# Optimization experiments

Hardware: AMD Instinct MI355X
Metric: run time of the kernel (lower is better)

Reference implementation:

```python
import jax, jax.numpy as jnp
import numpy as np

B, N, K, D, H, L = 2, 2048, 256, 768, 256, 64
REL_PROP = 3
NUM_BUCKETS = 64


def _pair_scores(u, dist_feat, left_w, left_b, right_w, right_b, out_w, out_b):
    # OptFFpairs-style pairwise scorer: left(u)_i + right(u)_j + dist_emb -> relu -> out
    left = jnp.einsum('bkd,hd->bkh', u, left_w) + left_b    # [B,K,H]
    right = jnp.einsum('bkd,hd->bkh', u, right_w) + right_b  # [B,K,H]
    h = jax.nn.relu(left[:, :, None, :] + right[:, None, :, :] + dist_feat)  # [B,K,K,H]
    return jnp.einsum('bijh,lh->bijl', h, out_w) + out_b     # [B,K,K,L]


def setup_inputs():
    key = jax.random.key(0)
    ks = jax.random.split(key, 12)
    s = 0.02
    all_span_vecs = jax.random.normal(ks[0], (B, N, D), dtype=jnp.float32)
    span_vecs = jax.random.normal(ks[1], (B, K, D), dtype=jnp.float32)
    span_begin = jnp.sort(jax.random.randint(ks[2], (B, K), 0, 1000), axis=-1).astype(jnp.int32)
    span_end = (span_begin + jax.random.randint(ks[3], (B, K), 1, 16)).astype(jnp.int32)
    square_mask = jnp.ones((B, K, K), dtype=jnp.float32)
    span_lengths = jnp.full((B,), float(K), dtype=jnp.float32)
    prune_indices = jnp.stack([
        jnp.sort(jax.random.choice(jax.random.fold_in(ks[4], b), N, (K,), replace=False))
        for b in range(B)
    ]).astype(jnp.int32)
    return {
        'all_span_vecs': all_span_vecs, 'span_vecs': span_vecs,
        'span_begin': span_begin, 'span_end': span_end,
        'square_mask': square_mask, 'span_lengths': span_lengths,
        'prune_indices': prune_indices,
        'left_w': jax.random.normal(ks[5], (H, D)) * s, 'left_b': jnp.zeros((H,), jnp.float32),
        'right_w': jax.random.normal(ks[6], (H, D)) * s, 'right_b': jnp.zeros((H,), jnp.float32),
        'dist_emb': jax.random.normal(ks[7], (NUM_BUCKETS, H)) * s,
        'out_w': jax.random.normal(ks[8], (L, H)) * s, 'out_b': jnp.zeros((L,), jnp.float32),
        'A_w': jax.random.normal(ks[9], (D, L)) * s,
        'B_w': jax.random.normal(ks[10], (D, L)) * s,
        'gate_w': jax.random.normal(ks[11], (D, 2 * D)) * s, 'gate_b': jnp.zeros((D,), jnp.float32),
    }


def reference(all_span_vecs, span_vecs, span_begin, span_end, square_mask, span_lengths,
              prune_indices, left_w, left_b, right_w, right_b, dist_emb, out_w, out_b,
              A_w, B_w, gate_w, gate_b):
    # distance-bucket embedding of the span pair (span_pair_generator)
    dist = span_begin[:, None, :] - span_end[:, :, None]                 # [B,K,K]
    buckets = jnp.clip(jnp.abs(dist), 0, NUM_BUCKETS - 1)
    dist_feat = dist_emb[buckets]                                        # [B,K,K,H]
    inv_len = 1.0 / span_lengths[:, None, None]                          # [B,1,1]

    update = span_vecs
    scores = _pair_scores(update, dist_feat, left_w, left_b, right_w, right_b, out_w, out_b)
    for _ in range(REL_PROP):
        probs = jax.nn.sigmoid(scores) * square_mask[..., None]          # [B,K,K,L]
        # torch: (A(probs) * update.unsqueeze(-2)).sum(-3) -> sum over i (rows)
        ctxt1 = jnp.einsum('bijl,dl,bid->bjd', probs, A_w, update) * inv_len
        # torch: (B(probs) * update.unsqueeze(-3)).sum(-2) -> sum over j (cols)
        ctxt2 = jnp.einsum('bijl,dl,bjd->bid', probs, B_w, update) * inv_len
        c = ctxt1 + ctxt2
        # MyGate: sigmoid-gated convex combination of old state and context
        g = jax.nn.sigmoid(jnp.concatenate([update, c], axis=-1) @ gate_w.T + gate_b)
        update = g * update + (1.0 - g) * c
        scores = _pair_scores(update, dist_feat, left_w, left_b, right_w, right_b, out_w, out_b)

    # overwrite_spans: scatter updated filtered spans back into the full span tensor
    valid = jnp.arange(K)[None, :] < span_lengths[:, None]               # [B,K]
    old = jnp.take_along_axis(all_span_vecs, prune_indices[..., None], axis=1)
    vals = jnp.where(valid[..., None], update, old)
    bidx = jnp.arange(B)[:, None]
    new_all = all_span_vecs.at[bidx, prune_indices].set(vals)
    return new_all, update, scores
```

## Files before the change

### kernel.cpp

```cpp
#include <hip/hip_runtime.h>

#define B_ 2
#define N_ 2048
#define K_ 256
#define D_ 768
#define H_ 256
#define L_ 64
#define BK_ (B_*K_)

typedef __attribute__((ext_vector_type(8))) __bf16 bf16x8;
typedef __attribute__((ext_vector_type(8))) unsigned short ushort8;
typedef __attribute__((ext_vector_type(4))) unsigned short ushort4v;
typedef __attribute__((ext_vector_type(4))) float f32x4;

__device__ __forceinline__ float sigm(float x) { return 1.0f / (1.0f + __expf(-x)); }

__device__ __forceinline__ unsigned short f2b(float f) {
    union { float f; unsigned int u; } v; v.f = f;
    unsigned int u = v.u;
    return (unsigned short)((u + 0x7FFFu + ((u >> 16) & 1u)) >> 16);
}
__device__ __forceinline__ unsigned short f2bc(float f) {
    __bf16 h = (__bf16)f;
    return __builtin_bit_cast(unsigned short, h);
}
__device__ __forceinline__ float b2f(unsigned short us) {
    union { unsigned int u; float f; } v; v.u = ((unsigned int)us) << 16;
    return v.f;
}
__device__ __forceinline__ bf16x8 ldb(const unsigned short* p) {
    ushort8 v = *(const ushort8*)p;
    return __builtin_bit_cast(bf16x8, v);
}
__device__ __forceinline__ bf16x8 cvt8(const float* p) {
    float4 v0 = *(const float4*)p;
    float4 v1 = *(const float4*)(p + 4);
    ushort8 u;
    u[0] = f2b(v0.x); u[1] = f2b(v0.y); u[2] = f2b(v0.z); u[3] = f2b(v0.w);
    u[4] = f2b(v1.x); u[5] = f2b(v1.y); u[6] = f2b(v1.z); u[7] = f2b(v1.w);
    return __builtin_bit_cast(bf16x8, u);
}

__global__ __launch_bounds__(256) void conv_all(
    const float* __restrict__ lw, const float* __restrict__ rw,
    const float* __restrict__ ow, const float* __restrict__ gw,
    const float* __restrict__ aw, const float* __restrict__ bw,
    const float* __restrict__ sv,
    unsigned short* __restrict__ lwb, unsigned short* __restrict__ rwb,
    unsigned short* __restrict__ owb, unsigned short* __restrict__ gwb,
    unsigned short* __restrict__ wab, unsigned short* __restrict__ wbb,
    unsigned short* __restrict__ ub)
{
    int i4 = (blockIdx.x * 256 + threadIdx.x) * 4;
    const float* src; unsigned short* dst; int off;
    if      (i4 <  196608) { src = lw; dst = lwb; off = 0; }
    else if (i4 <  393216) { src = rw; dst = rwb; off = 196608; }
    else if (i4 <  409600) { src = ow; dst = owb; off = 393216; }
    else if (i4 < 1589248) { src = gw; dst = gwb; off = 409600; }
    else if (i4 < 1638400) { src = aw; dst = wab; off = 1589248; }
    else if (i4 < 1687552) { src = bw; dst = wbb; off = 1638400; }
    else if (i4 < 2080768) { src = sv; dst = ub;  off = 1687552; }
    else return;
    int j = i4 - off;
    float4 v = *(const float4*)&src[j];
    ushort4v p; p.x = f2b(v.x); p.y = f2b(v.y); p.z = f2b(v.z); p.w = f2b(v.w);
    *(ushort4v*)&dst[j] = p;
}

__global__ __launch_bounds__(64) void lr_mfma(
    const unsigned short* __restrict__ Ub,
    const unsigned short* __restrict__ lwb, const float* __restrict__ lb,
    const unsigned short* __restrict__ rwb, const float* __restrict__ rb,
    float* __restrict__ outL, float* __restrict__ outR)
{
    const int side = blockIdx.z;
    const unsigned short* __restrict__ W = side ? rwb : lwb;
    const float* __restrict__ bias = side ? rb : lb;
    float* __restrict__ outp = side ? outR : outL;
    const int r0 = blockIdx.x * 16, n0 = blockIdx.y * 64;
    const int lane = threadIdx.x;
    const int col = lane & 15, quad = lane >> 4;
    const unsigned short* arow = &Ub[(size_t)(r0 + col)*D_ + quad*8];
    f32x4 acc[4] = {};
    #pragma unroll 4
    for (int kc = 0; kc < D_; kc += 32) {
        bf16x8 a = ldb(arow + kc);
        #pragma unroll
        for (int nt = 0; nt < 4; ++nt) {
            bf16x8 bb = ldb(&W[(size_t)(n0 + nt*16 + col)*D_ + kc + quad*8]);
            acc[nt] = __builtin_amdgcn_mfma_f32_16x16x32_bf16(a, bb, acc[nt], 0, 0, 0);
        }
    }
    #pragma unroll
    for (int nt = 0; nt < 4; ++nt) {
        const int n = n0 + nt*16 + col;
        const float bv = bias[n];
        #pragma unroll
        for (int r = 0; r < 4; ++r) {
            const size_t idx = (size_t)(r0 + quad*4 + r)*H_ + n;
            outp[idx] = acc[nt][r] + bv;
        }
    }
}

__global__ __launch_bounds__(256, 1) void scores_v8(
    const float* __restrict__ leftb, const float* __restrict__ rightb,
    const int* __restrict__ span_begin, const int* __restrict__ span_end,
    const float* __restrict__ de, const unsigned short* __restrict__ owb,
    const float* __restrict__ out_b, const float* __restrict__ mask,
    float* __restrict__ S, unsigned short* __restrict__ Pt, int writeP)
{
    const int j0 = blockIdx.x * 64;
    const int i0 = blockIdx.y * 8;
    const int b  = blockIdx.z;
    const int tid = threadIdx.x;
    const int w = tid >> 6, lane = tid & 63, col = lane & 15, quad = lane >> 4;
    const int jrow = w*16 + col;

    __shared__ float sL[8][256];
    __shared__ float sT[64][68];
    __shared__ float sMask[8][64];
    __shared__ int   sBkt[8][64];

    #pragma unroll
    for (int q = 0; q < 2; ++q) {
        int p = tid + q*256;
        int ii = p >> 6, jj = p & 63;
        int d = span_begin[b*K_ + j0 + jj] - span_end[b*K_ + i0 + ii];
        if (d < 0) d = -d;
        sBkt[ii][jj] = d > 63 ? 63 : d;
        sMask[ii][jj] = mask[(size_t)(b*K_ + i0 + ii)*K_ + j0 + jj];
    }
    #pragma unroll
    for (int q = 0; q < 2; ++q) {
        int f = tid + q*256;
        int row = f >> 6, c4 = (f & 63) * 4;
        *(float4*)&sL[row][c4] = *(const float4*)&leftb[(size_t)(b*K_ + i0 + row)*H_ + c4];
    }
    __syncthreads();

    int deoff[8];
    #pragma unroll
    for (int i = 0; i < 8; ++i) deoff[i] = sBkt[i][jrow] * H_;

    const float* rrow = &rightb[(size_t)(b*K_ + j0 + jrow)*H_ + quad*8];

    f32x4 acc[8][4] = {};
    #pragma unroll
    for (int k = 0; k < 8; ++k) {
        const float4 r0 = *(const float4*)&rrow[k*32];
        const float4 r1 = *(const float4*)&rrow[k*32 + 4];
        bf16x8 bbk[4];
        #pragma unroll
        for (int lt = 0; lt < 4; ++lt)
            bbk[lt] = ldb(&owb[(size_t)(lt*16 + col)*H_ + k*32 + quad*8]);
        #pragma unroll
        for (int i = 0; i < 8; ++i) {
            const float* dr = &de[deoff[i] + k*32 + quad*8];
            const float4 d0 = *(const float4*)dr;
            const float4 d1 = *(const float4*)(dr + 4);
            const float* lr = &sL[i][k*32 + quad*8];
            const float4 l0 = *(const float4*)lr;
            const float4 l1 = *(const float4*)(lr + 4);
            bf16x8 a;
            a[0] = (__bf16)fmaxf(0.f, l0.x + r0.x + d0.x);
            a[1] = (__bf16)fmaxf(0.f, l0.y + r0.y + d0.y);
            a[2] = (__bf16)fmaxf(0.f, l0.z + r0.z + d0.z);
            a[3] = (__bf16)fmaxf(0.f, l0.w + r0.w + d0.w);
            a[4] = (__bf16)fmaxf(0.f, l1.x + r1.x + d1.x);
            a[5] = (__bf16)fmaxf(0.f, l1.y + r1.y + d1.y);
            a[6] = (__bf16)fmaxf(0.f, l1.z + r1.z + d1.z);
            a[7] = (__bf16)fmaxf(0.f, l1.w + r1.w + d1.w);
            #pragma unroll
            for (int lt = 0; lt < 4; ++lt)
                acc[i][lt] = __builtin_amdgcn_mfma_f32_16x16x32_bf16(a, bbk[lt], acc[i][lt], 0, 0, 0);
        }
    }

    float ob[4];
    #pragma unroll
    for (int lt = 0; lt < 4; ++lt) ob[lt] = out_b[lt*16 + col];

    #pragma unroll
    for (int i = 0; i < 8; ++i) {
        __syncthreads();
        #pragma unroll
        for (int lt = 0; lt < 4; ++lt)
            #pragma unroll
            for (int r = 0; r < 4; ++r)
                sT[w*16 + quad*4 + r][lt*16 + col] = acc[i][lt][r] + ob[lt];
        __syncthreads();
        const int jj = tid >> 2, seg = (tid & 3) * 16;
        const int j = j0 + jj, ii = i0 + i;
        if (writeP) {
            const float msk = sMask[i][jj];
            ushort8 o0, o1;
            #pragma unroll
            for (int e = 0; e < 8; ++e) {
                o0[e] = f2bc(sigm(sT[jj][seg + e]) * msk);
                o1[e] = f2bc(sigm(sT[jj][seg + 8 + e]) * msk);
            }
            unsigned short* dst = &Pt[(((size_t)b*K_ + j)*K_ + ii)*L_ + seg];
            *(ushort8*)&dst[0] = o0;
            *(ushort8*)&dst[8] = o1;
        } else {
            float* dst = &S[(((size_t)b*K_ + ii)*K_ + j)*L_ + seg];
            #pragma unroll
            for (int q2 = 0; q2 < 4; ++q2) {
                float4 v;
                v.x = sT[jj][seg + q2*4 + 0];
                v.y = sT[jj][seg + q2*4 + 1];
                v.z = sT[jj][seg + q2*4 + 2];
                v.w = sT[jj][seg + q2*4 + 3];
                *(float4*)&dst[q2*4] = v;
            }
        }
    }
}

__global__ __launch_bounds__(512, 4) void ctxt_v4(
    const unsigned short* __restrict__ Pt, const float* __restrict__ U,
    const unsigned short* __restrict__ WAb, const unsigned short* __restrict__ WBb,
    const float* __restrict__ lens, float* __restrict__ cacc)
{
    const int bid = blockIdx.x;
    const int m0 = (bid & 15) << 4;
    const int t0 = ((bid >> 4) & 7) << 5;
    const int mode = (bid >> 7) & 1;
    const int b = bid >> 8;
    const unsigned short* __restrict__ Wb = mode ? WBb : WAb;
    const int tid = threadIdx.x;
    const int w = tid >> 6, lane = tid & 63, col = lane & 15, quad = lane >> 4;
    const int dbase = w * 96;

    __shared__ unsigned short sP[2][16][72];
    __shared__ float sU[2][768];

    bf16x8 bw[6][2];
    #pragma unroll
    for (int dt = 0; dt < 6; ++dt)
        #pragma unroll
        for (int kc = 0; kc < 2; ++kc)
            bw[dt][kc] = ldb(&Wb[(size_t)(dbase + dt*16 + col)*L_ + kc*32 + quad*8]);

    const bool doP = tid < 128;
    const bool doU = (tid >= 128) && (tid < 320);
    const int prow = (tid & 127) >> 3, pseg = (tid & 7) * 8;
    const int ucol = (tid - 128) * 4;
    size_t pbase, tstep;
    if (mode) { pbase = (((size_t)b*K_ + t0)*K_ + m0 + prow)*L_ + pseg; tstep = (size_t)K_*L_; }
    else      { pbase = (((size_t)b*K_ + m0 + prow)*K_ + t0)*L_ + pseg; tstep = (size_t)L_; }

    ushort8 pv; float4 uv;
    if (doP) pv = *(const ushort8*)&Pt[pbase];
    if (doU) uv = *(const float4*)&U[((size_t)b*K_ + t0)*D_ + ucol];

    f32x4 acc[6] = {};
    for (int t = 0; t < 32; ++t) {
        unsigned short (*bp)[72] = sP[t & 1];
        float* bu = sU[t & 1];
        if (doP) *(ushort8*)&bp[prow][pseg] = pv;
        if (doU) *(float4*)&bu[ucol] = uv;
        if (t < 31) {
            if (doP) pv = *(const ushort8*)&Pt[pbase + (size_t)(t + 1)*tstep];
            if (doU) uv = *(const float4*)&U[((size_t)b*K_ + t0 + t + 1)*D_ + ucol];
        }
        __syncthreads();
        bf16x8 a0 = ldb(&bp[col][quad*8]);
        bf16x8 a1 = ldb(&bp[col][32 + quad*8]);
        #pragma unroll
        for (int dt = 0; dt < 6; ++dt) {
            f32x4 g = {0.f, 0.f, 0.f, 0.f};
            g = __builtin_amdgcn_mfma_f32_16x16x32_bf16(a0, bw[dt][0], g, 0, 0, 0);
            g = __builtin_amdgcn_mfma_f32_16x16x32_bf16(a1, bw[dt][1], g, 0, 0, 0);
            const float uu = bu[dbase + dt*16 + col];
            acc[dt] += g * uu;
        }
    }

    const float inv_len = 1.0f / lens[b];
    #pragma unroll
    for (int dt = 0; dt < 6; ++dt)
        #pragma unroll
        for (int r = 0; r < 4; ++r) {
            const int m = m0 + quad*4 + r;
            atomicAdd(&cacc[((size_t)(b*K_) + m)*D_ + dbase + dt*16 + col],
                      acc[dt][r] * inv_len);
        }
}

__global__ __launch_bounds__(64) void gate_mfma(
    const unsigned short* __restrict__ Ub, const unsigned short* __restrict__ gwb,
    const float* __restrict__ gb,
    const float* __restrict__ Ucur, const float* __restrict__ Cc,
    float* __restrict__ Unext, unsigned short* __restrict__ Ubnext)
{
    const int r0 = blockIdx.x * 16, n0 = blockIdx.y * 64;
    const int lane = threadIdx.x;
    const int col = lane & 15, quad = lane >> 4;
    const unsigned short* arow_u = &Ub[(size_t)(r0 + col)*D_ + quad*8];
    const float* arow_c = &Cc[(size_t)(r0 + col)*D_ + quad*8];
    f32x4 acc[4] = {};
    #pragma unroll 4
    for (int kc = 0; kc < D_; kc += 32) {
        bf16x8 a = ldb(arow_u + kc);
        #pragma unroll
        for (int nt = 0; nt < 4; ++nt) {
            bf16x8 bb = ldb(&gwb[(size_t)(n0 + nt*16 + col)*(2*D_) + kc + quad*8]);
            acc[nt] = __builtin_amdgcn_mfma_f32_16x16x32_bf16(a, bb, acc[nt], 0, 0, 0);
        }
    }
    #pragma unroll 4
    for (int kc = 0; kc < D_; kc += 32) {
        bf16x8 a = cvt8(arow_c + kc);
        #pragma unroll
        for (int nt = 0; nt < 4; ++nt) {
            bf16x8 bb = ldb(&gwb[(size_t)(n0 + nt*16 + col)*(2*D_) + D_ + kc + quad*8]);
            acc[nt] = __builtin_amdgcn_mfma_f32_16x16x32_bf16(a, bb, acc[nt], 0, 0, 0);
        }
    }
    #pragma unroll
    for (int nt = 0; nt < 4; ++nt) {
        const int n = n0 + nt*16 + col;
        const float gbv = gb[n];
        #pragma unroll
        for (int r = 0; r < 4; ++r) {
            const size_t idx = (size_t)(r0 + quad*4 + r)*D_ + n;
            const float gg = sigm(acc[nt][r] + gbv);
            const float o = gg * Ucur[idx] + (1.f - gg) * Cc[idx];
            Unext[idx] = o;
            Ubnext[idx] = f2b(o);
        }
    }
}

__global__ __launch_bounds__(256) void scatter_kernel(
    const float* __restrict__ upd, const int* __restrict__ prune,
    const float* __restrict__ lens, float* __restrict__ out_all)
{
    const int blk = blockIdx.x;
    const int b = blk / K_, k = blk % K_;
    if ((float)k < lens[b]) {
        const int pi = prune[b*K_ + k];
        const int tid = threadIdx.x;
        if (tid < D_/4) {
            float4 v = *(const float4*)&upd[((size_t)b*K_ + k)*D_ + tid*4];
            *(float4*)&out_all[((size_t)b*N_ + pi)*D_ + tid*4] = v;
        }
    }
}

extern "C" void kernel_launch(void* const* d_in, const int* in_sizes, int n_in,
                              void* d_out, int out_size, void* d_ws, size_t ws_size,
                              hipStream_t stream) {
    (void)in_sizes; (void)n_in; (void)out_size; (void)ws_size;
    const float* all_span_vecs = (const float*)d_in[0];
    const float* span_vecs     = (const float*)d_in[1];
    const int*   span_begin    = (const int*)d_in[2];
    const int*   span_end      = (const int*)d_in[3];
    const float* mask          = (const float*)d_in[4];
    const float* lens          = (const float*)d_in[5];
    const int*   prune         = (const int*)d_in[6];
    const float* lw  = (const float*)d_in[7];
    const float* lb  = (const float*)d_in[8];
    const float* rw  = (const float*)d_in[9];
    const float* rb  = (const float*)d_in[10];
    const float* dist_emb = (const float*)d_in[11];
    const float* out_w    = (const float*)d_in[12];
    const float* out_b    = (const float*)d_in[13];
    const float* A_w = (const float*)d_in[14];
    const float* B_w = (const float*)d_in[15];
    const float* gw  = (const float*)d_in[16];
    const float* gb  = (const float*)d_in[17];

    float* out_all = (float*)d_out;
    float* out_upd = out_all + (size_t)B_*N_*D_;
    float* out_sc  = out_upd + (size_t)BK_*D_;

    float* ws     = (float*)d_ws;
    float* leftb  = ws;
    float* rightf = leftb + (size_t)BK_*H_;
    float* U0     = rightf + (size_t)BK_*H_;
    float* U1     = U0 + (size_t)BK_*D_;
    float* cbuf   = U1 + (size_t)BK_*D_;
    unsigned short* WAb = (unsigned short*)(cbuf + (size_t)BK_*D_);
    unsigned short* WBb = WAb + (size_t)D_*L_;
    unsigned short* lwb = WBb + (size_t)D_*L_;
    unsigned short* rwb = lwb + (size_t)H_*D_;
    unsigned short* owb = rwb + (size_t)H_*D_;
    unsigned short* gwb = owb + (size_t)L_*H_;
    unsigned short* Ub0 = gwb + (size_t)D_*2*D_;
    unsigned short* Ub1 = Ub0 + (size_t)BK_*D_;
    unsigned short* Pt  = Ub1 + (size_t)BK_*D_;

    hipMemcpyAsync(out_all, all_span_vecs, sizeof(float)*(size_t)B_*N_*D_,
                   hipMemcpyDeviceToDevice, stream);

    dim3 blk256(256), blk64(64), blk512(512);
    conv_all<<<dim3(2032), blk256, 0, stream>>>(lw, rw, out_w, gw, A_w, B_w, span_vecs,
                                                lwb, rwb, owb, gwb, WAb, WBb, Ub0);
    lr_mfma<<<dim3(BK_/16, H_/64, 2), blk64, 0, stream>>>(Ub0, lwb, lb, rwb, rb, leftb, rightf);
    scores_v8<<<dim3(K_/64, K_/8, B_), blk256, 0, stream>>>(leftb, rightf, span_begin, span_end,
                                                            dist_emb, owb, out_b, mask,
                                                            out_sc, Pt, 1);
    const float* Ucur = span_vecs;
    const unsigned short* Ubcur = Ub0;
    float* nexts[3] = {U0, U1, out_upd};
    unsigned short* nextsUb[3] = {Ub1, Ub0, Ub1};
    for (int it = 0; it < 3; ++it) {
        hipMemsetAsync(cbuf, 0, sizeof(float)*(size_t)BK_*D_, stream);
        ctxt_v4<<<dim3(512), blk512, 0, stream>>>(Pt, Ucur, WAb, WBb, lens, cbuf);
        gate_mfma<<<dim3(BK_/16, D_/64), blk64, 0, stream>>>(Ubcur, gwb, gb,
                                                             Ucur, cbuf, nexts[it], nextsUb[it]);
        Ucur = nexts[it];
        Ubcur = nextsUb[it];
        lr_mfma<<<dim3(BK_/16, H_/64, 2), blk64, 0, stream>>>(Ubcur, lwb, lb, rwb, rb, leftb, rightf);
        scores_v8<<<dim3(K_/64, K_/8, B_), blk256, 0, stream>>>(leftb, rightf, span_begin, span_end,
                                                                dist_emb, owb, out_b, mask,
                                                                out_sc, Pt, it == 2 ? 0 : 1);
    }
    scatter_kernel<<<dim3(BK_), blk256, 0, stream>>>(out_upd, prune, lens, out_all);
}
```

Measured before the change: 449.2 us.

## Stage bf16 distance embeddings in LDS and batch four steps per ctxt sync

The distance-embedding table is converted to bf16 once in the conversion kernel. The scores kernel then stages the whole table in shared memory, so the per-bucket gathers read LDS instead of global memory, and its launch bound now asks for two blocks per CU. The context kernel is restructured to load four reduction steps of P and U per barrier, with P laid out in MFMA fragment order, which cuts the number of syncs by four. The trade-offs are a larger LDS footprint, a possible register squeeze under the tighter launch bound, and extra bf16 rounding of the distance embeddings.

After: 1.532 ms. 3.41x slower.

```diff
diff --git a/kernel.cpp b/kernel.cpp
--- a/kernel.cpp
+++ b/kernel.cpp
@@ -45,11 +45,11 @@
     const float* __restrict__ lw, const float* __restrict__ rw,
     const float* __restrict__ ow, const float* __restrict__ gw,
     const float* __restrict__ aw, const float* __restrict__ bw,
-    const float* __restrict__ sv,
+    const float* __restrict__ sv, const float* __restrict__ de,
     unsigned short* __restrict__ lwb, unsigned short* __restrict__ rwb,
     unsigned short* __restrict__ owb, unsigned short* __restrict__ gwb,
     unsigned short* __restrict__ wab, unsigned short* __restrict__ wbb,
-    unsigned short* __restrict__ ub)
+    unsigned short* __restrict__ ub, unsigned short* __restrict__ deb)
 {
     int i4 = (blockIdx.x * 256 + threadIdx.x) * 4;
     const float* src; unsigned short* dst; int off;
@@ -60,6 +60,7 @@
     else if (i4 < 1638400) { src = aw; dst = wab; off = 1589248; }
     else if (i4 < 1687552) { src = bw; dst = wbb; off = 1638400; }
     else if (i4 < 2080768) { src = sv; dst = ub;  off = 1687552; }
+    else if (i4 < 2097152) { src = de; dst = deb; off = 2080768; }
     else return;
     int j = i4 - off;
     float4 v = *(const float4*)&src[j];
@@ -103,10 +104,10 @@
     }
 }
 
-__global__ __launch_bounds__(256, 1) void scores_v8(
+__global__ __launch_bounds__(256, 2) void scores_v9(
     const float* __restrict__ leftb, const float* __restrict__ rightb,
     const int* __restrict__ span_begin, const int* __restrict__ span_end,
-    const float* __restrict__ de, const unsigned short* __restrict__ owb,
+    const unsigned short* __restrict__ deb, const unsigned short* __restrict__ owb,
     const float* __restrict__ out_b, const float* __restrict__ mask,
     float* __restrict__ S, unsigned short* __restrict__ Pt, int writeP)
 {
@@ -117,11 +118,18 @@
     const int w = tid >> 6, lane = tid & 63, col = lane & 15, quad = lane >> 4;
     const int jrow = w*16 + col;
 
+    __shared__ unsigned short sDe[64][272];
     __shared__ float sL[8][256];
     __shared__ float sT[64][68];
     __shared__ float sMask[8][64];
     __shared__ int   sBkt[8][64];
 
+    #pragma unroll
+    for (int q = 0; q < 8; ++q) {
+        int c = tid + q*256;
+        int row = c >> 5, seg = (c & 31) * 8;
+        *(ushort8*)&sDe[row][seg] = *(const ushort8*)&deb[row*H_ + seg];
+    }
     #pragma unroll
     for (int q = 0; q < 2; ++q) {
         int p = tid + q*256;
@@ -139,9 +147,10 @@
     }
     __syncthreads();
 
+    const unsigned short* sDeF = &sDe[0][0];
     int deoff[8];
     #pragma unroll
-    for (int i = 0; i < 8; ++i) deoff[i] = sBkt[i][jrow] * H_;
+    for (int i = 0; i < 8; ++i) deoff[i] = sBkt[i][jrow] * 272;
 
     const float* rrow = &rightb[(size_t)(b*K_ + j0 + jrow)*H_ + quad*8];
 
@@ -156,21 +165,19 @@
             bbk[lt] = ldb(&owb[(size_t)(lt*16 + col)*H_ + k*32 + quad*8]);
         #pragma unroll
         for (int i = 0; i < 8; ++i) {
-            const float* dr = &de[deoff[i] + k*32 + quad*8];
-            const float4 d0 = *(const float4*)dr;
-            const float4 d1 = *(const float4*)(dr + 4);
+            const ushort8 dv = *(const ushort8*)&sDeF[deoff[i] + k*32 + quad*8];
             const float* lr = &sL[i][k*32 + quad*8];
             const float4 l0 = *(const float4*)lr;
             const float4 l1 = *(const float4*)(lr + 4);
             bf16x8 a;
-            a[0] = (__bf16)fmaxf(0.f, l0.x + r0.x + d0.x);
-            a[1] = (__bf16)fmaxf(0.f, l0.y + r0.y + d0.y);
-            a[2] = (__bf16)fmaxf(0.f, l0.z + r0.z + d0.z);
-            a[3] = (__bf16)fmaxf(0.f, l0.w + r0.w + d0.w);
-            a[4] = (__bf16)fmaxf(0.f, l1.x + r1.x + d1.x);
-            a[5] = (__bf16)fmaxf(0.f, l1.y + r1.y + d1.y);
-            a[6] = (__bf16)fmaxf(0.f, l1.z + r1.z + d1.z);
-            a[7] = (__bf16)fmaxf(0.f, l1.w + r1.w + d1.w);
+            a[0] = (__bf16)fmaxf(0.f, l0.x + r0.x + b2f(dv[0]));
+            a[1] = (__bf16)fmaxf(0.f, l0.y + r0.y + b2f(dv[1]));
+            a[2] = (__bf16)fmaxf(0.f, l0.z + r0.z + b2f(dv[2]));
+            a[3] = (__bf16)fmaxf(0.f, l0.w + r0.w + b2f(dv[3]));
+            a[4] = (__bf16)fmaxf(0.f, l1.x + r1.x + b2f(dv[4]));
+            a[5] = (__bf16)fmaxf(0.f, l1.y + r1.y + b2f(dv[5]));
+            a[6] = (__bf16)fmaxf(0.f, l1.z + r1.z + b2f(dv[6]));
+            a[7] = (__bf16)fmaxf(0.f, l1.w + r1.w + b2f(dv[7]));
             #pragma unroll
             for (int lt = 0; lt < 4; ++lt)
                 acc[i][lt] = __builtin_amdgcn_mfma_f32_16x16x32_bf16(a, bbk[lt], acc[i][lt], 0, 0, 0);
@@ -218,7 +225,7 @@
     }
 }
 
-__global__ __launch_bounds__(512, 4) void ctxt_v4(
+__global__ __launch_bounds__(512, 4) void ctxt_v5(
     const unsigned short* __restrict__ Pt, const float* __restrict__ U,
     const unsigned short* __restrict__ WAb, const unsigned short* __restrict__ WBb,
     const float* __restrict__ lens, float* __restrict__ cacc)
@@ -233,8 +240,8 @@
     const int w = tid >> 6, lane = tid & 63, col = lane & 15, quad = lane >> 4;
     const int dbase = w * 96;
 
-    __shared__ unsigned short sP[2][16][72];
-    __shared__ float sU[2][768];
+    __shared__ unsigned short sPf[2][4][1024];
+    __shared__ float sU[2][3072];
 
     bf16x8 bw[6][2];
     #pragma unroll
@@ -243,38 +250,52 @@
         for (int kc = 0; kc < 2; ++kc)
             bw[dt][kc] = ldb(&Wb[(size_t)(dbase + dt*16 + col)*L_ + kc*32 + quad*8]);
 
-    const bool doP = tid < 128;
-    const bool doU = (tid >= 128) && (tid < 320);
-    const int prow = (tid & 127) >> 3, pseg = (tid & 7) * 8;
-    const int ucol = (tid - 128) * 4;
-    size_t pbase, tstep;
-    if (mode) { pbase = (((size_t)b*K_ + t0)*K_ + m0 + prow)*L_ + pseg; tstep = (size_t)K_*L_; }
-    else      { pbase = (((size_t)b*K_ + m0 + prow)*K_ + t0)*L_ + pseg; tstep = (size_t)L_; }
-
-    ushort8 pv; float4 uv;
-    if (doP) pv = *(const ushort8*)&Pt[pbase];
-    if (doU) uv = *(const float4*)&U[((size_t)b*K_ + t0)*D_ + ucol];
+    const int ptt   = tid >> 7;
+    const int pc    = tid & 127;
+    const int prow  = pc & 15;
+    const int pfrag = pc >> 4;
+    const int pkc   = pfrag >> 2;
+    const int pquad = pfrag & 3;
+    const int pdst  = pkc*512 + (pquad*16 + prow)*8;
+    const int pseg  = pfrag * 8;
+    size_t pRowBase, pTstep;
+    if (mode) { pRowBase = ((size_t)(b*K_)*K_ + m0 + prow)*L_ + pseg;  pTstep = (size_t)K_*L_; }
+    else      { pRowBase = ((size_t)(b*K_ + m0 + prow)*K_)*L_ + pseg;  pTstep = (size_t)L_; }
+
+    const int utt0 = tid / 192, uc0 = (tid % 192) * 4;
+    const int uf1  = 512 + tid;
+    const int utt1 = uf1 / 192, uc1 = (uf1 % 192) * 4;
+
+    ushort8 pv = *(const ushort8*)&Pt[pRowBase + (size_t)(t0 + ptt)*pTstep];
+    float4 uv0 = *(const float4*)&U[((size_t)b*K_ + t0 + utt0)*D_ + uc0];
+    float4 uv1;
+    if (tid < 256) uv1 = *(const float4*)&U[((size_t)b*K_ + t0 + utt1)*D_ + uc1];
 
     f32x4 acc[6] = {};
-    for (int t = 0; t < 32; ++t) {
-        unsigned short (*bp)[72] = sP[t & 1];
-        float* bu = sU[t & 1];
-        if (doP) *(ushort8*)&bp[prow][pseg] = pv;
-        if (doU) *(float4*)&bu[ucol] = uv;
-        if (t < 31) {
-            if (doP) pv = *(const ushort8*)&Pt[pbase + (size_t)(t + 1)*tstep];
-            if (doU) uv = *(const float4*)&U[((size_t)b*K_ + t0 + t + 1)*D_ + ucol];
-        }
+    for (int p = 0; p < 8; ++p) {
+        const int cur = p & 1;
+        *(ushort8*)&sPf[cur][ptt][pdst] = pv;
+        *(float4*)&sU[cur][utt0*768 + uc0] = uv0;
+        if (tid < 256) *(float4*)&sU[cur][utt1*768 + uc1] = uv1;
         __syncthreads();
-        bf16x8 a0 = ldb(&bp[col][quad*8]);
-        bf16x8 a1 = ldb(&bp[col][32 + quad*8]);
-        #pragma unroll
-        for (int dt = 0; dt < 6; ++dt) {
-            f32x4 g = {0.f, 0.f, 0.f, 0.f};
-            g = __builtin_amdgcn_mfma_f32_16x16x32_bf16(a0, bw[dt][0], g, 0, 0, 0);
-            g = __builtin_amdgcn_mfma_f32_16x16x32_bf16(a1, bw[dt][1], g, 0, 0, 0);
-            const float uu = bu[dbase + dt*16 + col];
-            acc[dt] += g * uu;
+        if (p < 7) {
+            const int tn = t0 + (p + 1)*4;
+            pv  = *(const ushort8*)&Pt[pRowBase + (size_t)(tn + ptt)*pTstep];
+            uv0 = *(const float4*)&U[((size_t)b*K_ + tn + utt0)*D_ + uc0];
+            if (tid < 256) uv1 = *(const float4*)&U[((size_t)b*K_ + tn + utt1)*D_ + uc1];
+        }
+        #pragma unroll
+        for (int tt = 0; tt < 4; ++tt) {
+            bf16x8 a0 = ldb(&sPf[cur][tt][lane*8]);
+            bf16x8 a1 = ldb(&sPf[cur][tt][512 + lane*8]);
+            #pragma unroll
+            for (int dt = 0; dt < 6; ++dt) {
+                f32x4 g = {0.f, 0.f, 0.f, 0.f};
+                g = __builtin_amdgcn_mfma_f32_16x16x32_bf16(a0, bw[dt][0], g, 0, 0, 0);
+                g = __builtin_amdgcn_mfma_f32_16x16x32_bf16(a1, bw[dt][1], g, 0, 0, 0);
+                const float uu = sU[cur][tt*768 + dbase + dt*16 + col];
+                acc[dt] += g * uu;
+            }
         }
     }
 
@@ -389,7 +410,8 @@
     unsigned short* rwb = lwb + (size_t)H_*D_;
     unsigned short* owb = rwb + (size_t)H_*D_;
     unsigned short* gwb = owb + (size_t)L_*H_;
-    unsigned short* Ub0 = gwb + (size_t)D_*2*D_;
+    unsigned short* deb = gwb + (size_t)D_*2*D_;
+    unsigned short* Ub0 = deb + (size_t)64*H_;
     unsigned short* Ub1 = Ub0 + (size_t)BK_*D_;
     unsigned short* Pt  = Ub1 + (size_t)BK_*D_;
 
@@ -397,11 +419,11 @@
                    hipMemcpyDeviceToDevice, stream);
 
     dim3 blk256(256), blk64(64), blk512(512);
-    conv_all<<<dim3(2032), blk256, 0, stream>>>(lw, rw, out_w, gw, A_w, B_w, span_vecs,
-                                                lwb, rwb, owb, gwb, WAb, WBb, Ub0);
+    conv_all<<<dim3(2048), blk256, 0, stream>>>(lw, rw, out_w, gw, A_w, B_w, span_vecs, dist_emb,
+                                                lwb, rwb, owb, gwb, WAb, WBb, Ub0, deb);
     lr_mfma<<<dim3(BK_/16, H_/64, 2), blk64, 0, stream>>>(Ub0, lwb, lb, rwb, rb, leftb, rightf);
-    scores_v8<<<dim3(K_/64, K_/8, B_), blk256, 0, stream>>>(leftb, rightf, span_begin, span_end,
-                                                            dist_emb, owb, out_b, mask,
+    scores_v9<<<dim3(K_/64, K_/8, B_), blk256, 0, stream>>>(leftb, rightf, span_begin, span_end,
+                                                            deb, owb, out_b, mask,
                                                             out_sc, Pt, 1);
     const float* Ucur = span_vecs;
     const unsigned short* Ubcur = Ub0;
@@ -409,14 +431,14 @@
     unsigned short* nextsUb[3] = {Ub1, Ub0, Ub1};
     for (int it = 0; it < 3; ++it) {
         hipMemsetAsync(cbuf, 0, sizeof(float)*(size_t)BK_*D_, stream);
-        ctxt_v4<<<dim3(512), blk512, 0, stream>>>(Pt, Ucur, WAb, WBb, lens, cbuf);
+        ctxt_v5<<<dim3(512), blk512, 0, stream>>>(Pt, Ucur, WAb, WBb, lens, cbuf);
         gate_mfma<<<dim3(BK_/16, D_/64), blk64, 0, stream>>>(Ubcur, gwb, gb,
                                                              Ucur, cbuf, nexts[it], nextsUb[it]);
         Ucur = nexts[it];
         Ubcur = nextsUb[it];
         lr_mfma<<<dim3(BK_/16, H_/64, 2), blk64, 0, stream>>>(Ubcur, lwb, lb, rwb, rb, leftb, rightf);
-        scores_v8<<<dim3(K_/64, K_/8, B_), blk256, 0, stream>>>(leftb, rightf, span_begin, span_end,
-                                                                dist_emb, owb, out_b, mask,
+        scores_v9<<<dim3(K_/64, K_/8, B_), blk256, 0, stream>>>(leftb, rightf, span_begin, span_end,
+                                                                deb, owb, out_b, mask,
                                                                 out_sc, Pt, it == 2 ? 0 : 1);
     }
     scatter_kernel<<<dim3(BK_), blk256, 0, stream>>>(out_upd, prune, lens, out_all);
```

## Stage bf16 distance embeddings in LDS and move ctxt prefetch after barrier

Applied to the files above, without the earlier changes.

Converts dist_emb to bf16 in the conversion pass, and each scores block now loads the whole 64x256 table into padded shared memory. This replaces scattered global float4 gathers per (i,j) with LDS reads, and launch bounds now allow two blocks per CU. The ctxt kernel issues its next-tile global prefetch after the barrier rather than before it, which changes how the prefetch overlaps with the MFMA work. The cost is extra LDS (~35KB per block), an extra bf16 rounding of the distance embedding, and a larger conversion launch.

Result: faster. 439.4 us (-2.2%).

```diff
diff --git a/kernel.cpp b/kernel.cpp
--- a/kernel.cpp
+++ b/kernel.cpp
@@ -45,11 +45,11 @@
     const float* __restrict__ lw, const float* __restrict__ rw,
     const float* __restrict__ ow, const float* __restrict__ gw,
     const float* __restrict__ aw, const float* __restrict__ bw,
-    const float* __restrict__ sv,
+    const float* __restrict__ sv, const float* __restrict__ de,
     unsigned short* __restrict__ lwb, unsigned short* __restrict__ rwb,
     unsigned short* __restrict__ owb, unsigned short* __restrict__ gwb,
     unsigned short* __restrict__ wab, unsigned short* __restrict__ wbb,
-    unsigned short* __restrict__ ub)
+    unsigned short* __restrict__ ub, unsigned short* __restrict__ deb)
 {
     int i4 = (blockIdx.x * 256 + threadIdx.x) * 4;
     const float* src; unsigned short* dst; int off;
@@ -60,6 +60,7 @@
     else if (i4 < 1638400) { src = aw; dst = wab; off = 1589248; }
     else if (i4 < 1687552) { src = bw; dst = wbb; off = 1638400; }
     else if (i4 < 2080768) { src = sv; dst = ub;  off = 1687552; }
+    else if (i4 < 2097152) { src = de; dst = deb; off = 2080768; }
     else return;
     int j = i4 - off;
     float4 v = *(const float4*)&src[j];
@@ -103,10 +104,10 @@
     }
 }
 
-__global__ __launch_bounds__(256, 1) void scores_v8(
+__global__ __launch_bounds__(256, 2) void scores_v9(
     const float* __restrict__ leftb, const float* __restrict__ rightb,
     const int* __restrict__ span_begin, const int* __restrict__ span_end,
-    const float* __restrict__ de, const unsigned short* __restrict__ owb,
+    const unsigned short* __restrict__ deb, const unsigned short* __restrict__ owb,
     const float* __restrict__ out_b, const float* __restrict__ mask,
     float* __restrict__ S, unsigned short* __restrict__ Pt, int writeP)
 {
@@ -117,11 +118,18 @@
     const int w = tid >> 6, lane = tid & 63, col = lane & 15, quad = lane >> 4;
     const int jrow = w*16 + col;
 
+    __shared__ unsigned short sDe[64][272];
     __shared__ float sL[8][256];
     __shared__ float sT[64][68];
     __shared__ float sMask[8][64];
     __shared__ int   sBkt[8][64];
 
+    #pragma unroll
+    for (int q = 0; q < 8; ++q) {
+        int c = tid + q*256;
+        int row = c >> 5, seg = (c & 31) * 8;
+        *(ushort8*)&sDe[row][seg] = *(const ushort8*)&deb[row*H_ + seg];
+    }
     #pragma unroll
     for (int q = 0; q < 2; ++q) {
         int p = tid + q*256;
@@ -139,9 +147,10 @@
     }
     __syncthreads();
 
+    const unsigned short* sDeF = &sDe[0][0];
     int deoff[8];
     #pragma unroll
-    for (int i = 0; i < 8; ++i) deoff[i] = sBkt[i][jrow] * H_;
+    for (int i = 0; i < 8; ++i) deoff[i] = sBkt[i][jrow] * 272;
 
     const float* rrow = &rightb[(size_t)(b*K_ + j0 + jrow)*H_ + quad*8];
 
@@ -156,21 +165,19 @@
             bbk[lt] = ldb(&owb[(size_t)(lt*16 + col)*H_ + k*32 + quad*8]);
         #pragma unroll
         for (int i = 0; i < 8; ++i) {
-            const float* dr = &de[deoff[i] + k*32 + quad*8];
-            const float4 d0 = *(const float4*)dr;
-            const float4 d1 = *(const float4*)(dr + 4);
+            const ushort8 dv = *(const ushort8*)&sDeF[deoff[i] + k*32 + quad*8];
             const float* lr = &sL[i][k*32 + quad*8];
             const float4 l0 = *(const float4*)lr;
             const float4 l1 = *(const float4*)(lr + 4);
             bf16x8 a;
-            a[0] = (__bf16)fmaxf(0.f, l0.x + r0.x + d0.x);
-            a[1] = (__bf16)fmaxf(0.f, l0.y + r0.y + d0.y);
-            a[2] = (__bf16)fmaxf(0.f, l0.z + r0.z + d0.z);
-            a[3] = (__bf16)fmaxf(0.f, l0.w + r0.w + d0.w);
-            a[4] = (__bf16)fmaxf(0.f, l1.x + r1.x + d1.x);
-            a[5] = (__bf16)fmaxf(0.f, l1.y + r1.y + d1.y);
-            a[6] = (__bf16)fmaxf(0.f, l1.z + r1.z + d1.z);
-            a[7] = (__bf16)fmaxf(0.f, l1.w + r1.w + d1.w);
+            a[0] = (__bf16)fmaxf(0.f, l0.x + r0.x + b2f(dv[0]));
+            a[1] = (__bf16)fmaxf(0.f, l0.y + r0.y + b2f(dv[1]));
+            a[2] = (__bf16)fmaxf(0.f, l0.z + r0.z + b2f(dv[2]));
+            a[3] = (__bf16)fmaxf(0.f, l0.w + r0.w + b2f(dv[3]));
+            a[4] = (__bf16)fmaxf(0.f, l1.x + r1.x + b2f(dv[4]));
+            a[5] = (__bf16)fmaxf(0.f, l1.y + r1.y + b2f(dv[5]));
+            a[6] = (__bf16)fmaxf(0.f, l1.z + r1.z + b2f(dv[6]));
+            a[7] = (__bf16)fmaxf(0.f, l1.w + r1.w + b2f(dv[7]));
             #pragma unroll
             for (int lt = 0; lt < 4; ++lt)
                 acc[i][lt] = __builtin_amdgcn_mfma_f32_16x16x32_bf16(a, bbk[lt], acc[i][lt], 0, 0, 0);
@@ -218,7 +225,7 @@
     }
 }
 
-__global__ __launch_bounds__(512, 4) void ctxt_v4(
+__global__ __launch_bounds__(512, 4) void ctxt_v6(
     const unsigned short* __restrict__ Pt, const float* __restrict__ U,
     const unsigned short* __restrict__ WAb, const unsigned short* __restrict__ WBb,
     const float* __restrict__ lens, float* __restrict__ cacc)
@@ -261,11 +268,11 @@
         float* bu = sU[t & 1];
         if (doP) *(ushort8*)&bp[prow][pseg] = pv;
         if (doU) *(float4*)&bu[ucol] = uv;
+        __syncthreads();
         if (t < 31) {
             if (doP) pv = *(const ushort8*)&Pt[pbase + (size_t)(t + 1)*tstep];
             if (doU) uv = *(const float4*)&U[((size_t)b*K_ + t0 + t + 1)*D_ + ucol];
         }
-        __syncthreads();
         bf16x8 a0 = ldb(&bp[col][quad*8]);
         bf16x8 a1 = ldb(&bp[col][32 + quad*8]);
         #pragma unroll
@@ -389,7 +396,8 @@
     unsigned short* rwb = lwb + (size_t)H_*D_;
     unsigned short* owb = rwb + (size_t)H_*D_;
     unsigned short* gwb = owb + (size_t)L_*H_;
-    unsigned short* Ub0 = gwb + (size_t)D_*2*D_;
+    unsigned short* deb = gwb + (size_t)D_*2*D_;
+    unsigned short* Ub0 = deb + (size_t)64*H_;
     unsigned short* Ub1 = Ub0 + (size_t)BK_*D_;
     unsigned short* Pt  = Ub1 + (size_t)BK_*D_;
 
@@ -397,11 +405,11 @@
                    hipMemcpyDeviceToDevice, stream);
 
     dim3 blk256(256), blk64(64), blk512(512);
-    conv_all<<<dim3(2032), blk256, 0, stream>>>(lw, rw, out_w, gw, A_w, B_w, span_vecs,
-                                                lwb, rwb, owb, gwb, WAb, WBb, Ub0);
+    conv_all<<<dim3(2048), blk256, 0, stream>>>(lw, rw, out_w, gw, A_w, B_w, span_vecs, dist_emb,
+                                                lwb, rwb, owb, gwb, WAb, WBb, Ub0, deb);
     lr_mfma<<<dim3(BK_/16, H_/64, 2), blk64, 0, stream>>>(Ub0, lwb, lb, rwb, rb, leftb, rightf);
-    scores_v8<<<dim3(K_/64, K_/8, B_), blk256, 0, stream>>>(leftb, rightf, span_begin, span_end,
-                                                            dist_emb, owb, out_b, mask,
+    scores_v9<<<dim3(K_/64, K_/8, B_), blk256, 0, stream>>>(leftb, rightf, span_begin, span_end,
+                                                            deb, owb, out_b, mask,
                                                             out_sc, Pt, 1);
     const float* Ucur = span_vecs;
     const unsigned short* Ubcur = Ub0;
@@ -409,14 +417,14 @@
     unsigned short* nextsUb[3] = {Ub1, Ub0, Ub1};
     for (int it = 0; it < 3; ++it) {
         hipMemsetAsync(cbuf, 0, sizeof(float)*(size_t)BK_*D_, stream);
-        ctxt_v4<<<dim3(512), blk512, 0, stream>>>(Pt, Ucur, WAb, WBb, lens, cbuf);
+        ctxt_v6<<<dim3(512), blk512, 0, stream>>>(Pt, Ucur, WAb, WBb, lens, cbuf);
         gate_mfma<<<dim3(BK_/16, D_/64), blk64, 0, stream>>>(Ubcur, gwb, gb,
                                                              Ucur, cbuf, nexts[it], nextsUb[it]);
         Ucur = nexts[it];
         Ubcur = nextsUb[it];
         lr_mfma<<<dim3(BK_/16, H_/64, 2), blk64, 0, stream>>>(Ubcur, lwb, lb, rwb, rb, leftb, rightf);
-        scores_v8<<<dim3(K_/64, K_/8, B_), blk256, 0, stream>>>(leftb, rightf, span_begin, span_end,
-                                                                dist_emb, owb, out_b, mask,
+        scores_v9<<<dim3(K_/64, K_/8, B_), blk256, 0, stream>>>(leftb, rightf, span_begin, span_end,
+                                                                deb, owb, out_b, mask,
                                                                 out_sc, Pt, it == 2 ? 0 : 1);
     }
     scatter_kernel<<<dim3(BK_), blk256, 0, stream>>>(out_upd, prune, lens, out_all);
```
